# Performance work log

Hardware: AMD Instinct MI355X
Metric: run time of the kernel (lower is better)

## Reference

```python
import jax, jax.numpy as jnp
import numpy as np
import math

B, HW, C, HEADS = 32, 784, 384, 8
T = HW + 1            # 785 tokens incl. cls
TP = HW // 4 + 1      # 197 tokens after pooling
FF = 4 * C
EPS = 1e-5


def _ln2d(x, w, b):
    # nn.LayerNorm over last two dims (tokens, channels) with affine params
    mu = x.mean(axis=(-2, -1), keepdims=True)
    var = x.var(axis=(-2, -1), keepdims=True)
    return (x - mu) / jnp.sqrt(var + EPS) * w + b


def setup_inputs() -> dict:
    key = jax.random.key(0)
    ks = jax.random.split(key, 10)
    sc = math.sqrt(2.0 / C)  # kaiming-ish scale
    rn = lambda k, sh, s=1.0: (jax.random.normal(k, sh, jnp.float32) * s)
    return {
        "x": rn(ks[0], (B, HW, C)),
        "cls_token": rn(ks[1], (B, 1, C)),
        "w_ln1": jnp.ones((T, C), jnp.float32),
        "b_ln1": jnp.zeros((T, C), jnp.float32),
        "Wq": rn(ks[2], (C, C), sc),
        "Wk": rn(ks[3], (C, C), sc),
        "Wv": rn(ks[4], (C, C), sc),
        "Wo": rn(ks[5], (C, C), sc),
        "w_ln2": jnp.ones((TP, C), jnp.float32),
        "b_ln2": jnp.zeros((TP, C), jnp.float32),
        "W1": rn(ks[6], (FF, C), sc),
        "W2": rn(ks[7], (C, FF), math.sqrt(2.0 / FF)),
    }


def reference(x, cls_token, w_ln1, b_ln1, Wq, Wk, Wv, Wo, w_ln2, b_ln2, W1, W2):
    d = C // HEADS
    x_in = jnp.concatenate([cls_token, x], axis=1)           # (B,T,C)
    x1 = _ln2d(x_in, w_ln1, b_ln1)
    # MHSA (dropout disabled for determinism)
    q = (x1 @ Wq.T).reshape(B, T, HEADS, d)
    k = (x1 @ Wk.T).reshape(B, T, HEADS, d)
    v = (x1 @ Wv.T).reshape(B, T, HEADS, d)
    attn = jax.nn.softmax(jnp.einsum('bqhd,bkhd->bhqk', q, k) / math.sqrt(d), axis=-1)
    x_mhsa = jnp.einsum('bhqk,bkhd->bqhd', attn, v).reshape(B, T, C) @ Wo.T
    x_res1 = x_in + x_mhsa
    # Pooling block: channel importance from mean-pooled edge aggregation
    nodes = x_res1[:, 1:]                                     # (B,HW,C)
    ci = jax.nn.sigmoid(x_mhsa.mean(axis=1))                  # (B,C)  AvgPool1d(kernel=T)
    ca = jnp.einsum('bnc,bc->bn', nodes, ci)                  # (B,HW) channel aggregation
    idx = jnp.argsort(ca, axis=1)                             # ascending, like torch.sort
    nodes_sorted = jnp.take_along_axis(nodes, idx[:, :, None], axis=1)
    nodes_pooled = nodes_sorted[:, (HW // 4) * 3:]            # keep top quarter (largest ca)
    x2 = jnp.concatenate([x_res1[:, 0:1], nodes_pooled], axis=1)  # (B,TP,C)
    x2n = _ln2d(x2, w_ln2, b_ln2)
    # MLP (exact-erf GELU, as F.gelu default)
    h = jax.nn.gelu(x2n @ W1.T, approximate=False) @ W2.T
    x_res2 = x2n + h
    return x_res2[:, 1:], x_res2[:, 0:1]
```

## Files before the change

### kernel.cpp

```cpp
#include <hip/hip_runtime.h>
#include <hip/hip_bf16.h>
#include <math.h>

typedef __hip_bfloat16 bf16;
typedef _Float16 f16;
typedef __attribute__((ext_vector_type(8))) _Float16 f16x8;
typedef __attribute__((ext_vector_type(4))) _Float16 f16x4;
typedef __attribute__((ext_vector_type(4))) float f32x4;

#define B_ 32
#define HW_ 784
#define T_ 785
#define TP_ 197
#define C_ 384
#define H_ 8
#define D_ 48
#define FF_ 1536

#define MFMA16(a, b, c) __builtin_amdgcn_mfma_f32_16x16x32_f16(a, b, c, 0, 0, 0)

static constexpr size_t NRES = (size_t)B_ * T_ * C_;
static constexpr size_t NX   = (size_t)B_ * HW_ * C_;
static constexpr size_t NCLS = (size_t)B_ * C_;
static constexpr size_t NLN1 = (size_t)T_ * C_;
static constexpr size_t NWP  = (size_t)C_ * C_;
static constexpr size_t NLN2 = (size_t)TP_ * C_;
static constexpr size_t NW1  = (size_t)FF_ * C_;
static constexpr size_t NX2  = (size_t)B_ * TP_ * C_;
static constexpr size_t NH   = (size_t)B_ * TP_ * FF_;

static constexpr size_t NX1F = (size_t)1576 * 12 * 512;
static constexpr size_t NQKF = (size_t)256 * 56 * 2 * 512;
static constexpr size_t NVF  = (size_t)256 * 3 * 25 * 512;
static constexpr size_t NX2F = (size_t)400 * 12 * 512;
static constexpr size_t NHF  = (size_t)400 * 48 * 512;

static constexpr size_t XF_OFF   = 0;
static constexpr size_t CLSF_OFF = XF_OFF   + NX   * 4;
static constexpr size_t LN1W_OFF = CLSF_OFF + NCLS * 4;
static constexpr size_t LN1B_OFF = LN1W_OFF + NLN1 * 4;
static constexpr size_t WQF_OFF  = LN1B_OFF + NLN1 * 4;
static constexpr size_t LN2W_OFF = WQF_OFF  + 4 * NWP * 4;
static constexpr size_t LN2B_OFF = LN2W_OFF + NLN2 * 4;
static constexpr size_t W1F_OFF  = LN2B_OFF + NLN2 * 4;
static constexpr size_t W2F_OFF  = W1F_OFF  + NW1  * 4;
static constexpr size_t X1H_OFF  = W2F_OFF  + NW1  * 4;
static constexpr size_t X1L_OFF  = X1H_OFF  + NX1F * 2;
static constexpr size_t QFH_OFF  = X1L_OFF  + NX1F * 2;
static constexpr size_t QFL_OFF  = QFH_OFF  + NQKF * 2;
static constexpr size_t KFH_OFF  = QFL_OFF  + NQKF * 2;
static constexpr size_t KFL_OFF  = KFH_OFF  + NQKF * 2;
static constexpr size_t VFH_OFF  = KFL_OFF  + NQKF * 2;
static constexpr size_t VFL_OFF  = VFH_OFF  + NVF  * 2;
static constexpr size_t ATH_OFF  = VFL_OFF  + NVF  * 2;
static constexpr size_t ATL_OFF  = ATH_OFF  + NX1F * 2;
static constexpr size_t XM_OFF   = ATL_OFF  + NX1F * 2;
static constexpr size_t RES_OFF  = XM_OFF   + NRES * 4;
static constexpr size_t X2N_OFF  = RES_OFF  + NRES * 4;
static constexpr size_t X2NH_OFF = X2N_OFF  + NX2  * 4;
static constexpr size_t X2NL_OFF = X2NH_OFF + NX2F * 2;
static constexpr size_t HFH_OFF  = X2NL_OFF + NX2F * 2;
static constexpr size_t HFL_OFF  = HFH_OFF  + NHF  * 2;
static constexpr size_t WPH_OFF  = HFL_OFF  + NHF  * 2;
static constexpr size_t WPL_OFF  = WPH_OFF  + 4 * NWP * 2;
static constexpr size_t WFH_OFF  = WPL_OFF  + 4 * NWP * 2;
static constexpr size_t WFL_OFF  = WFH_OFF  + 2 * NW1 * 2;
static constexpr size_t MU_OFF   = WFL_OFF  + 2 * NW1 * 2;
static constexpr size_t RS_OFF   = MU_OFF   + 128;
static constexpr size_t CID_OFF  = RS_OFF   + 128;
static constexpr size_t CAD_OFF  = CID_OFF  + NCLS * 8;
static constexpr size_t PERM_OFF = CAD_OFF  + (size_t)B_ * HW_ * 8;
static constexpr size_t FLAG_OFF = PERM_OFF + (size_t)B_ * (TP_ - 1) * 4;
static constexpr size_t PS_OFF   = FLAG_OFF + 16;
static constexpr size_t CIP_OFF  = PS_OFF + 32 * 16 * 16;
static constexpr size_t L2PS_OFF = CIP_OFF + (size_t)B_ * 8 * C_ * 8;
static constexpr size_t L2MU_OFF = L2PS_OFF + 32 * 8 * 16;
static constexpr size_t L2RS_OFF = L2MU_OFF + 128;
static constexpr size_t PART_OFF = L2RS_OFF + 128;
static constexpr size_t ARENA_BYTES = PART_OFF + 2 * NX2 * 4;

__device__ __align__(256) unsigned char g_arena[ARENA_BYTES];

template <typename Tp>
__device__ __forceinline__ Tp* ap(size_t off) { return (Tp*)(g_arena + off); }

__device__ __forceinline__ void splitf(float v, f16& h, f16& l)
{
    float a = fabsf(v);
    f16 hv = (a >= 6.103515625e-05f) ? (f16)v : (f16)0.f;
    h = hv;
    l = (f16)((v - (float)hv) * 4096.f);
}

__device__ __forceinline__ size_t afrag(int row, int c, int KC)
{
    return ((size_t)((row >> 4) * KC + (c >> 5)) << 9)
         + (size_t)(((row & 15) | (((c >> 3) & 3) << 4)) << 3) + (c & 7);
}

__global__ void detect_kernel(const unsigned* __restrict__ w)
{
    if (threadIdx.x == 0)
        *ap<int>(FLAG_OFF) = (w[0] == 0x3F803F80u) ? 1 : 0;
}

struct SrcPtrs { const void* p[12]; };
static constexpr size_t SEGB[13] = {
    0,
    NX,
    NX + NCLS,
    NX + NCLS + NLN1,
    NX + NCLS + 2 * NLN1,
    NX + NCLS + 2 * NLN1 + NWP,
    NX + NCLS + 2 * NLN1 + 2 * NWP,
    NX + NCLS + 2 * NLN1 + 3 * NWP,
    NX + NCLS + 2 * NLN1 + 4 * NWP,
    NX + NCLS + 2 * NLN1 + 4 * NWP + NLN2,
    NX + NCLS + 2 * NLN1 + 4 * NWP + 2 * NLN2,
    NX + NCLS + 2 * NLN1 + 4 * NWP + 2 * NLN2 + NW1,
    NX + NCLS + 2 * NLN1 + 4 * NWP + 2 * NLN2 + 2 * NW1,
};
static constexpr size_t NTOT_CVT = SEGB[12];

__global__ __launch_bounds__(256) void cvt_all_kernel(SrcPtrs sp)
{
    size_t i = (size_t)blockIdx.x * 256 + threadIdx.x;
    if (i >= NTOT_CVT) return;
    int seg = 0;
#pragma unroll
    for (int k = 1; k < 12; k++) seg += (i >= SEGB[k]);
    size_t li = i - SEGB[seg];
    const void* src = sp.p[seg];
    float v = (*ap<int>(FLAG_OFF))
        ? __bfloat162float(((const bf16*)src)[li])
        : ((const float*)src)[li];
    ap<float>(XF_OFF)[i] = v;
}

__global__ __launch_bounds__(256) void wrepack_kernel()
{
    size_t i = (size_t)blockIdx.x * 256 + threadIdx.x;
    const size_t n1 = 4 * NWP;
    if (i >= n1 + 2 * NW1) return;
    float v; f16 *oh, *ol;
    if (i < n1) {
        size_t u = i;
        int blk = (int)(u >> 9), le = (int)(u & 511);
        int l = le >> 3, e = le & 7;
        int nt = blk / 12, kc = blk - nt * 12;
        int n = nt * 16 + (l & 15), k = kc * 32 + ((l >> 4) << 3) + e;
        v = ap<float>(WQF_OFF)[(size_t)n * C_ + k];
        oh = ap<f16>(WPH_OFF) + i; ol = ap<f16>(WPL_OFF) + i;
    } else if (i < n1 + NW1) {
        size_t u = i - n1;
        int blk = (int)(u >> 9), le = (int)(u & 511);
        int l = le >> 3, e = le & 7;
        int nt = blk / 12, kc = blk - nt * 12;
        int n = nt * 16 + (l & 15), k = kc * 32 + ((l >> 4) << 3) + e;
        v = ap<float>(W1F_OFF)[(size_t)n * C_ + k];
        oh = ap<f16>(WFH_OFF) + u; ol = ap<f16>(WFL_OFF) + u;
    } else {
        size_t u = i - n1 - NW1;
        int blk = (int)(u >> 9), le = (int)(u & 511);
        int l = le >> 3, e = le & 7;
        int nt = blk / 48, kc = blk - nt * 48;
        int n = nt * 16 + (l & 15), k = kc * 32 + ((l >> 4) << 3) + e;
        v = ap<float>(W2F_OFF)[(size_t)n * FF_ + k];
        oh = ap<f16>(WFH_OFF) + NW1 + u; ol = ap<f16>(WFL_OFF) + NW1 + u;
    }
    f16 h, lo; splitf(v, h, lo);
    *oh = h; *ol = lo;
}

__device__ __forceinline__ float xin_val(int b, int t, int c)
{
    return (t == 0) ? ap<float>(CLSF_OFF)[b * C_ + c]
                    : ap<float>(XF_OFF)[((size_t)b * HW_ + (t - 1)) * C_ + c];
}

__global__ __launch_bounds__(256) void stats1a_kernel()
{
    const int TC = T_ * C_;
    const int SL = (TC + 15) / 16;
    int b = blockIdx.x, s = blockIdx.y, tid = threadIdx.x;
    int e0 = s * SL, e1 = min(e0 + SL, TC);
    __shared__ double r1[256], r2[256];
    double sm = 0.0, s2 = 0.0;
    for (int e = e0 + tid; e < e1; e += 256) {
        int t = e / C_, c = e - t * C_;
        double v = (double)xin_val(b, t, c);
        sm += v; s2 += v * v;
    }
    r1[tid] = sm; r2[tid] = s2; __syncthreads();
    for (int o = 128; o; o >>= 1) {
        if (tid < o) { r1[tid] += r1[tid + o]; r2[tid] += r2[tid + o]; }
        __syncthreads();
    }
    if (tid == 0) {
        double2* ps = ap<double2>(PS_OFF);
        ps[b * 16 + s] = make_double2(r1[0], r2[0]);
    }
}

__global__ __launch_bounds__(64) void stats1b_kernel()
{
    int b = blockIdx.x, lane = threadIdx.x;
    const double2* ps = ap<double2>(PS_OFF);
    double sm = 0.0, s2 = 0.0;
    if (lane < 16) { sm = ps[b * 16 + lane].x; s2 = ps[b * 16 + lane].y; }
    for (int o = 8; o; o >>= 1) { sm += __shfl_down(sm, o); s2 += __shfl_down(s2, o); }
    if (lane == 0) {
        const int TC = T_ * C_;
        double m = sm / TC;
        double var = s2 / TC - m * m;
        ap<float>(MU_OFF)[b] = (float)m;
        ap<float>(RS_OFF)[b] = (float)(1.0 / sqrt(var + 1e-5));
    }
}

__global__ __launch_bounds__(256) void ln1_apply_kernel()
{
    size_t i = (size_t)blockIdx.x * 256 + threadIdx.x;
    if (i >= NRES) return;
    int grow = (int)(i / C_);
    int c = (int)(i - (size_t)grow * C_);
    int b = grow / T_, t = grow - b * T_;
    float v = xin_val(b, t, c);
    float r = (v - ap<float>(MU_OFF)[b]) * ap<float>(RS_OFF)[b]
              * ap<float>(LN1W_OFF)[t * C_ + c]
              + ap<float>(LN1B_OFF)[t * C_ + c];
    f16 h, l; splitf(r, h, l);
    size_t off = afrag(grow, c, 12);
    ap<f16>(X1H_OFF)[off] = h;
    ap<f16>(X1L_OFF)[off] = l;
}

template<int EMODE>
__global__ __launch_bounds__(256, 2) void gemm_fd(
    size_t ah_off, size_t al_off, size_t bh_off, size_t bl_off,
    size_t c_off, int M, int N, int KC, int GY)
{
    int nwg = (int)gridDim.x;
    int lin = blockIdx.x;
    int q8 = nwg >> 3, r8 = nwg & 7, xcd = lin & 7, pos = lin >> 3;
    int wg = (xcd < r8 ? xcd * (q8 + 1) : r8 * (q8 + 1) + (xcd - r8) * q8) + pos;
    int bx = wg / GY, by = wg - bx * GY;
    int kbeg = 0, kend = KC;
    if (EMODE == 6) { int ks = KC >> 1; kbeg = blockIdx.z * ks; kend = kbeg + ks; }
    int tid = threadIdx.x, w = tid >> 6, l = tid & 63;
    int wmt = bx * 8 + (w >> 1) * 4;
    int wnt = by * 8 + (w & 1) * 4;
    const f16* gAh = ap<f16>(ah_off);
    const f16* gAl = ap<f16>(al_off);
    const f16* gBh = ap<f16>(bh_off);
    const f16* gBl = ap<f16>(bl_off);
    size_t ab = (size_t)wmt * KC * 512 + (size_t)l * 8;
    size_t bb = (size_t)wnt * KC * 512 + (size_t)l * 8;

    const f32x4 zf = {0.f, 0.f, 0.f, 0.f};
    f32x4 acc1[4][4], acc2[4][4];
#pragma unroll
    for (int i = 0; i < 4; i++)
#pragma unroll
        for (int j = 0; j < 4; j++) { acc1[i][j] = zf; acc2[i][j] = zf; }

    for (int kc = kbeg; kc < kend; kc++) {
        f16x8 fah[4], fal[4], fbh[4], fbl[4];
#pragma unroll
        for (int i = 0; i < 4; i++) {
            size_t ao = ab + (size_t)(i * KC + kc) * 512;
            size_t bo = bb + (size_t)(i * KC + kc) * 512;
            fah[i] = *(const f16x8*)(gAh + ao);
            fal[i] = *(const f16x8*)(gAl + ao);
            fbh[i] = *(const f16x8*)(gBh + bo);
            fbl[i] = *(const f16x8*)(gBl + bo);
        }
        __builtin_amdgcn_s_setprio(1);
#pragma unroll
        for (int i = 0; i < 4; i++)
#pragma unroll
            for (int j = 0; j < 4; j++) {
                acc1[i][j] = MFMA16(fah[i], fbh[j], acc1[i][j]);
                acc2[i][j] = MFMA16(fah[i], fbl[j], acc2[i][j]);
                acc2[i][j] = MFMA16(fal[i], fbh[j], acc2[i][j]);
            }
        __builtin_amdgcn_s_setprio(0);
    }

    int l4 = ((l >> 4) << 2), lr = l & 15;
#pragma unroll
    for (int i = 0; i < 4; i++) {
        int rowb = (wmt + i) * 16 + l4;
#pragma unroll
        for (int j = 0; j < 4; j++) {
            int col = (wnt + j) * 16 + lr;
#pragma unroll
            for (int r = 0; r < 4; r++) {
                int row = rowb + r;
                if (row >= M) continue;
                float v = acc1[i][j][r] + acc2[i][j][r] * 0.000244140625f;
                if (EMODE == 5) {
                    int seg = col / C_;
                    int cn = col - seg * C_;
                    int hh = cn / D_, dd = cn - hh * D_;
                    int b2 = row / T_, t2 = row - b2 * T_;
                    int bh = b2 * H_ + hh;
                    float vv = (seg == 0) ? v * 0.14433756729740643f : v;
                    f16 h, lo; splitf(vv, h, lo);
                    if (seg < 2) {
                        size_t off = ((size_t)(bh * 112 + (t2 >> 4) * 2 + (dd >> 5)) << 9)
                                   + (size_t)(((t2 & 15) | (((dd >> 3) & 3) << 4)) << 3) + (dd & 7);
                        if (seg == 0) { ap<f16>(QFH_OFF)[off] = h; ap<f16>(QFL_OFF)[off] = lo; }
                        else          { ap<f16>(KFH_OFF)[off] = h; ap<f16>(KFL_OFF)[off] = lo; }
                    } else {
                        size_t off = ((size_t)(bh * 75 + (dd >> 4) * 25 + (t2 >> 5)) << 9)
                                   + (size_t)(((dd & 15) | (((t2 >> 3) & 3) << 4)) << 3) + (t2 & 7);
                        ap<f16>(VFH_OFF)[off] = h; ap<f16>(VFL_OFF)[off] = lo;
                    }
                } else if (EMODE == 4) {
                    ap<float>(c_off)[(size_t)row * N + col] = v;
                    int b2 = row / T_, t2 = row - b2 * T_;
                    ap<float>(RES_OFF)[(size_t)row * N + col] = v + xin_val(b2, t2, col);
                } else if (EMODE == 2) {
                    float g = 0.5f * v * (1.f + erff(v * 0.70710678f));
                    f16 h, lo; splitf(g, h, lo);
                    size_t off = afrag(row, col, 48);
                    ap<f16>(HFH_OFF)[off] = h;
                    ap<f16>(HFL_OFF)[off] = lo;
                } else {
                    ap<float>(PART_OFF)[(size_t)blockIdx.z * NX2 + (size_t)row * N + col] = v;
                }
            }
        }
    }
}

__global__ __launch_bounds__(256) void flash_kernel()
{
    __shared__ f16 Plds[4][2][2][16][40];
    int nwg = (int)gridDim.x;
    int lin = blockIdx.x;
    int q8 = nwg >> 3, r8 = nwg & 7, xcd = lin & 7, pos = lin >> 3;
    int wg = (xcd < r8 ? xcd * (q8 + 1) : r8 * (q8 + 1) + (xcd - r8) * q8) + pos;
    int bh = wg / 7, qblk = wg - bh * 7;
    int wv = threadIdx.x >> 6, l = threadIdx.x & 63;
    int qt0 = qblk * 8 + wv * 2;
    if (qt0 >= 50) return;
    int b = bh >> 3, h = bh & 7;
    size_t qkb = (size_t)bh * 57344;
    const f16* QH = ap<f16>(QFH_OFF) + qkb;
    const f16* QL = ap<f16>(QFL_OFF) + qkb;
    const f16* KH = ap<f16>(KFH_OFF) + qkb;
    const f16* KL = ap<f16>(KFL_OFF) + qkb;
    const f16* VH = ap<f16>(VFH_OFF) + (size_t)bh * 38400;
    const f16* VL = ap<f16>(VFL_OFF) + (size_t)bh * 38400;
    int myq = l & 15, g = l >> 4;

    f16x8 qh[2][2], ql[2][2];
#pragma unroll
    for (int u = 0; u < 2; u++)
#pragma unroll
        for (int kc = 0; kc < 2; kc++) {
            size_t qo = ((size_t)((qt0 + u) * 2 + kc) << 9) + (size_t)l * 8;
            qh[u][kc] = *(const f16x8*)(QH + qo);
            ql[u][kc] = *(const f16x8*)(QL + qo);
        }
    const f32x4 zf = {0.f, 0.f, 0.f, 0.f};
    f32x4 o1[2][3], o2[2][3];
#pragma unroll
    for (int u = 0; u < 2; u++)
#pragma unroll
        for (int j = 0; j < 3; j++) { o1[u][j] = zf; o2[u][j] = zf; }
    float mrun[2] = {-3e38f, -3e38f}, srun[2] = {0.f, 0.f};

    for (int w = 0; w < 25; w++) {
        f16x8 kh[2][2], kl[2][2];
#pragma unroll
        for (int kt2 = 0; kt2 < 2; kt2++)
#pragma unroll
            for (int kc = 0; kc < 2; kc++) {
                size_t ko = ((size_t)((w * 2 + kt2) * 2 + kc) << 9) + (size_t)l * 8;
                kh[kt2][kc] = *(const f16x8*)(KH + ko);
                kl[kt2][kc] = *(const f16x8*)(KL + ko);
            }
        f16x8 vh[3], vl[3];
#pragma unroll
        for (int j = 0; j < 3; j++) {
            size_t vo = ((size_t)(j * 25 + w) << 9) + (size_t)l * 8;
            vh[j] = *(const f16x8*)(VH + vo);
            vl[j] = *(const f16x8*)(VL + vo);
        }
#pragma unroll
        for (int u = 0; u < 2; u++) {
            f32x4 s1[2] = {zf, zf}, s2[2] = {zf, zf};
#pragma unroll
            for (int kt2 = 0; kt2 < 2; kt2++)
#pragma unroll
                for (int kc = 0; kc < 2; kc++) {
                    s1[kt2] = MFMA16(kh[kt2][kc], qh[u][kc], s1[kt2]);
                    s2[kt2] = MFMA16(kh[kt2][kc], ql[u][kc], s2[kt2]);
                    s2[kt2] = MFMA16(kl[kt2][kc], qh[u][kc], s2[kt2]);
                }
            float sv[8];
#pragma unroll
            for (int kt2 = 0; kt2 < 2; kt2++)
#pragma unroll
                for (int r = 0; r < 4; r++)
                    sv[kt2 * 4 + r] = s1[kt2][r] + s2[kt2][r] * 0.000244140625f;
            if (w == 24) {
#pragma unroll
                for (int kt2 = 0; kt2 < 2; kt2++)
#pragma unroll
                    for (int r = 0; r < 4; r++)
                        if (kt2 * 16 + g * 4 + r >= 17) sv[kt2 * 4 + r] = -1e30f;
            }
            float pm = sv[0];
#pragma unroll
            for (int j2 = 1; j2 < 8; j2++) pm = fmaxf(pm, sv[j2]);
            pm = fmaxf(pm, __shfl_xor(pm, 16));
            pm = fmaxf(pm, __shfl_xor(pm, 32));
            float mnew = fmaxf(mrun[u], pm);
            float pv[8]; float ls = 0.f;
#pragma unroll
            for (int j2 = 0; j2 < 8; j2++) { pv[j2] = __expf(sv[j2] - mnew); ls += pv[j2]; }
            ls += __shfl_xor(ls, 16);
            ls += __shfl_xor(ls, 32);
            if (__any(pm > mrun[u])) {
                float fac = __expf(mrun[u] - mnew);
                float fr[4];
#pragma unroll
                for (int r = 0; r < 4; r++) fr[r] = __shfl(fac, g * 4 + r);
#pragma unroll
                for (int j = 0; j < 3; j++)
#pragma unroll
                    for (int r = 0; r < 4; r++) { o1[u][j][r] *= fr[r]; o2[u][j][r] *= fr[r]; }
                srun[u] = srun[u] * fac + ls;
                mrun[u] = mnew;
            } else {
                srun[u] += ls;
            }
#pragma unroll
            for (int kt2 = 0; kt2 < 2; kt2++) {
                f16x4 hh, llo;
#pragma unroll
                for (int r = 0; r < 4; r++) { f16 a, bb2; splitf(pv[kt2 * 4 + r], a, bb2); hh[r] = a; llo[r] = bb2; }
                *(f16x4*)&Plds[wv][u][0][myq][kt2 * 16 + g * 4] = hh;
                *(f16x4*)&Plds[wv][u][1][myq][kt2 * 16 + g * 4] = llo;
            }
            f16x8 pah = *(const f16x8*)&Plds[wv][u][0][myq][g * 8];
            f16x8 pal = *(const f16x8*)&Plds[wv][u][1][myq][g * 8];
#pragma unroll
            for (int j = 0; j < 3; j++) {
                o1[u][j] = MFMA16(pah, vh[j], o1[u][j]);
                o2[u][j] = MFMA16(pah, vl[j], o2[u][j]);
                o2[u][j] = MFMA16(pal, vh[j], o2[u][j]);
            }
        }
    }
#pragma unroll
    for (int u = 0; u < 2; u++) {
        float inv = 1.f / srun[u];
        float ir[4];
#pragma unroll
        for (int r = 0; r < 4; r++) ir[r] = __shfl(inv, g * 4 + r);
#pragma unroll
        for (int j = 0; j < 3; j++) {
            int c = h * D_ + j * 16 + myq;
#pragma unroll
            for (int r = 0; r < 4; r++) {
                int q = (qt0 + u) * 16 + g * 4 + r;
                if (q >= T_) continue;
                float v = (o1[u][j][r] + o2[u][j][r] * 0.000244140625f) * ir[r];
                int grow = b * T_ + q;
                f16 hv, lv; splitf(v, hv, lv);
                size_t off = afrag(grow, c, 12);
                ap<f16>(ATH_OFF)[off] = hv;
                ap<f16>(ATL_OFF)[off] = lv;
            }
        }
    }
}

__global__ __launch_bounds__(384) void cia_kernel()
{
    int b = blockIdx.x, s = blockIdx.y, c = threadIdx.x;
    const float* xm = ap<float>(XM_OFF);
    const int SL = (T_ + 7) / 8;
    int t0 = s * SL, t1 = min(t0 + SL, T_);
    double sm = 0.0;
    for (int t = t0; t < t1; t++) sm += (double)xm[((size_t)b * T_ + t) * C_ + c];
    ap<double>(CIP_OFF)[((size_t)b * 8 + s) * C_ + c] = sm;
}

__global__ __launch_bounds__(384) void cib_kernel()
{
    int b = blockIdx.x, c = threadIdx.x;
    const double* pp = ap<double>(CIP_OFF);
    double sm = 0.0;
#pragma unroll
    for (int s = 0; s < 8; s++) sm += pp[((size_t)b * 8 + s) * C_ + c];
    sm /= (double)T_;
    ap<double>(CID_OFF)[b * C_ + c] = 1.0 / (1.0 + exp(-sm));
}

__global__ __launch_bounds__(64) void ca_kernel()
{
    const float* xres1 = ap<float>(RES_OFF);
    const double* ci   = ap<double>(CID_OFF);
    int idx = blockIdx.x;
    int b = idx / HW_, n = idx - b * HW_;
    int lane = threadIdx.x;
    double s = 0.0;
    for (int c = lane; c < C_; c += 64)
        s += (double)xres1[((size_t)b * T_ + 1 + n) * C_ + c] * ci[b * C_ + c];
    for (int o = 32; o; o >>= 1) s += __shfl_down(s, o);
    if (lane == 0) ap<double>(CAD_OFF)[idx] = s;
}

__global__ __launch_bounds__(256) void rank_kernel()
{
    const double* ca = ap<double>(CAD_OFF);
    int* perm = ap<int>(PERM_OFF);
    int b = blockIdx.x, tid = threadIdx.x;
    __shared__ double cs[HW_];
    for (int i = tid; i < HW_; i += 256) cs[i] = ca[b * HW_ + i];
    __syncthreads();
    for (int i = tid; i < HW_; i += 256) {
        double vi = cs[i];
        int r = 0;
        for (int j = 0; j < HW_; j++) {
            double vj = cs[j];
            r += (vj < vi) || (vj == vi && j < i);
        }
        if (r >= HW_ - TP_ + 1) perm[b * (TP_ - 1) + (r - (HW_ - TP_ + 1))] = i;
    }
}

__global__ __launch_bounds__(256) void ln2a_kernel()
{
    const float* xres1 = ap<float>(RES_OFF);
    const int* perm = ap<int>(PERM_OFF);
    const int TC = TP_ * C_;
    const int SL = (TC + 7) / 8;
    int b = blockIdx.x, s = blockIdx.y, tid = threadIdx.x;
    int e0 = s * SL, e1 = min(e0 + SL, TC);
    __shared__ double r1[256], r2[256];
    double sm = 0.0, s2 = 0.0;
    for (int e = e0 + tid; e < e1; e += 256) {
        int t = e / C_, c = e - t * C_;
        int st = (t == 0) ? 0 : 1 + perm[b * (TP_ - 1) + t - 1];
        double v = (double)xres1[((size_t)b * T_ + st) * C_ + c];
        sm += v; s2 += v * v;
    }
    r1[tid] = sm; r2[tid] = s2; __syncthreads();
    for (int o = 128; o; o >>= 1) {
        if (tid < o) { r1[tid] += r1[tid + o]; r2[tid] += r2[tid + o]; }
        __syncthreads();
    }
    if (tid == 0) {
        double2* ps = ap<double2>(L2PS_OFF);
        ps[b * 8 + s] = make_double2(r1[0], r2[0]);
    }
}

__global__ __launch_bounds__(64) void ln2b_kernel()
{
    int b = blockIdx.x, lane = threadIdx.x;
    const double2* ps = ap<double2>(L2PS_OFF);
    double sm = 0.0, s2 = 0.0;
    if (lane < 8) { sm = ps[b * 8 + lane].x; s2 = ps[b * 8 + lane].y; }
    for (int o = 4; o; o >>= 1) { sm += __shfl_down(sm, o); s2 += __shfl_down(s2, o); }
    if (lane == 0) {
        const int TC = TP_ * C_;
        double m = sm / TC;
        double var = s2 / TC - m * m;
        ap<float>(L2MU_OFF)[b] = (float)m;
        ap<float>(L2RS_OFF)[b] = (float)(1.0 / sqrt(var + 1e-5));
    }
}

__global__ __launch_bounds__(256) void ln2_apply_kernel()
{
    size_t i = (size_t)blockIdx.x * 256 + threadIdx.x;
    if (i >= NX2) return;
    const int TC = TP_ * C_;
    int b = (int)(i / TC);
    int e = (int)(i - (size_t)b * TC);
    int t = e / C_, c = e - t * C_;
    const int* perm = ap<int>(PERM_OFF);
    int st = (t == 0) ? 0 : 1 + perm[b * (TP_ - 1) + t - 1];
    float v = ap<float>(RES_OFF)[((size_t)b * T_ + st) * C_ + c];
    float r = (v - ap<float>(L2MU_OFF)[b]) * ap<float>(L2RS_OFF)[b]
              * ap<float>(LN2W_OFF)[e] + ap<float>(LN2B_OFF)[e];
    ap<float>(X2N_OFF)[i] = r;
    int grow = b * TP_ + t;
    f16 h, l; splitf(r, h, l);
    size_t off = afrag(grow, c, 12);
    ap<f16>(X2NH_OFF)[off] = h;
    ap<f16>(X2NL_OFF)[off] = l;
}

__global__ __launch_bounds__(256) void ffn2_reduce_kernel(float* __restrict__ out)
{
    const size_t tot = NX2;
    size_t i = (size_t)blockIdx.x * 256 + threadIdx.x;
    if (i >= tot) return;
    const float* part = ap<float>(PART_OFF);
    float v = part[i] + part[tot + i] + ap<float>(X2N_OFF)[i];
    int gm = (int)(i / C_);
    int gn = (int)(i - (size_t)gm * C_);
    int b = gm / TP_, t = gm - b * TP_;
    size_t off = (t == 0)
        ? ((size_t)B_ * (TP_ - 1) * C_ + (size_t)b * C_ + gn)
        : ((size_t)(b * (TP_ - 1) + (t - 1)) * C_ + gn);
    out[off] = v;
}

extern "C" void kernel_launch(void* const* d_in, const int* in_sizes, int n_in,
                              void* d_out, int out_size, void* d_ws, size_t ws_size,
                              hipStream_t stream)
{
    float* out = (float*)d_out;
    (void)d_ws; (void)ws_size; (void)in_sizes; (void)n_in; (void)out_size;

    const int M1 = B_ * T_;
    const int M2 = B_ * TP_;

    detect_kernel<<<1, 64, 0, stream>>>((const unsigned*)d_in[2]);
    SrcPtrs sp;
    for (int i = 0; i < 12; i++) sp.p[i] = d_in[i];
    cvt_all_kernel<<<(int)((NTOT_CVT + 255) / 256), 256, 0, stream>>>(sp);
    wrepack_kernel<<<(int)((4 * NWP + 2 * NW1 + 255) / 256), 256, 0, stream>>>();

    stats1a_kernel<<<dim3(B_, 16), 256, 0, stream>>>();
    stats1b_kernel<<<B_, 64, 0, stream>>>();
    ln1_apply_kernel<<<(int)((NRES + 255) / 256), 256, 0, stream>>>();

    gemm_fd<5><<<dim3(197 * 9), 256, 0, stream>>>(
        X1H_OFF, X1L_OFF, WPH_OFF, WPL_OFF, 0, M1, 3 * C_, 12, 9);

    flash_kernel<<<dim3(256 * 7), 256, 0, stream>>>();

    gemm_fd<4><<<dim3(197 * 3), 256, 0, stream>>>(
        ATH_OFF, ATL_OFF,
        WPH_OFF + (size_t)442368 * 2, WPL_OFF + (size_t)442368 * 2,
        XM_OFF, M1, C_, 12, 3);

    cia_kernel<<<dim3(B_, 8), 384, 0, stream>>>();
    cib_kernel<<<B_, 384, 0, stream>>>();
    ca_kernel<<<B_ * HW_, 64, 0, stream>>>();
    rank_kernel<<<B_, 256, 0, stream>>>();
    ln2a_kernel<<<dim3(B_, 8), 256, 0, stream>>>();
    ln2b_kernel<<<B_, 64, 0, stream>>>();
    ln2_apply_kernel<<<(int)((NX2 + 255) / 256), 256, 0, stream>>>();

    gemm_fd<2><<<dim3(50 * 12), 256, 0, stream>>>(
        X2NH_OFF, X2NL_OFF, WFH_OFF, WFL_OFF, 0, M2, FF_, 12, 12);
    gemm_fd<6><<<dim3(50 * 3, 1, 2), 256, 0, stream>>>(
        HFH_OFF, HFL_OFF, WFH_OFF + NW1 * 2, WFL_OFF + NW1 * 2, 0, M2, C_, 48, 3);
    ffn2_reduce_kernel<<<(int)((NX2 + 255) / 256), 256, 0, stream>>>(out);
}
```

Before: 912.8 us.

## Stream V tiles contiguously, add MFMA priority hints, and pack ca_kernel waves

Reorders the V fragment layout so each key window's three tiles sit next to each other, and walks K/V with incrementing pointers. s_setprio is raised around the MFMA bursts in the flash kernel. The max and sum reductions become trees, and the hi/lo split is inlined with a denormal cutoff. ca_kernel now runs four rows per 256-thread block instead of one per 64-thread block, which cuts launch and block overhead. The inlined split could differ slightly from splitf in rounding.

New measurement: 1.072 ms. 1.17x slower.

```diff
diff --git a/kernel.cpp b/kernel.cpp
--- a/kernel.cpp
+++ b/kernel.cpp
@@ -313,7 +313,7 @@
                         if (seg == 0) { ap<f16>(QFH_OFF)[off] = h; ap<f16>(QFL_OFF)[off] = lo; }
                         else          { ap<f16>(KFH_OFF)[off] = h; ap<f16>(KFL_OFF)[off] = lo; }
                     } else {
-                        size_t off = ((size_t)(bh * 75 + (dd >> 4) * 25 + (t2 >> 5)) << 9)
+                        size_t off = ((size_t)(bh * 75 + (t2 >> 5) * 3 + (dd >> 4)) << 9)
                                    + (size_t)(((dd & 15) | (((t2 >> 3) & 3) << 4)) << 3) + (t2 & 7);
                         ap<f16>(VFH_OFF)[off] = h; ap<f16>(VFL_OFF)[off] = lo;
                     }
@@ -350,10 +350,10 @@
     size_t qkb = (size_t)bh * 57344;
     const f16* QH = ap<f16>(QFH_OFF) + qkb;
     const f16* QL = ap<f16>(QFL_OFF) + qkb;
-    const f16* KH = ap<f16>(KFH_OFF) + qkb;
-    const f16* KL = ap<f16>(KFL_OFF) + qkb;
-    const f16* VH = ap<f16>(VFH_OFF) + (size_t)bh * 38400;
-    const f16* VL = ap<f16>(VFL_OFF) + (size_t)bh * 38400;
+    const f16* kptrH = ap<f16>(KFH_OFF) + qkb + (size_t)l * 8;
+    const f16* kptrL = ap<f16>(KFL_OFF) + qkb + (size_t)l * 8;
+    const f16* vptrH = ap<f16>(VFH_OFF) + (size_t)bh * 38400 + (size_t)l * 8;
+    const f16* vptrL = ap<f16>(VFL_OFF) + (size_t)bh * 38400 + (size_t)l * 8;
     int myq = l & 15, g = l >> 4;
 
     f16x8 qh[2][2], ql[2][2];
@@ -374,33 +374,34 @@
     float mrun[2] = {-3e38f, -3e38f}, srun[2] = {0.f, 0.f};
 
     for (int w = 0; w < 25; w++) {
-        f16x8 kh[2][2], kl[2][2];
-#pragma unroll
-        for (int kt2 = 0; kt2 < 2; kt2++)
-#pragma unroll
-            for (int kc = 0; kc < 2; kc++) {
-                size_t ko = ((size_t)((w * 2 + kt2) * 2 + kc) << 9) + (size_t)l * 8;
-                kh[kt2][kc] = *(const f16x8*)(KH + ko);
-                kl[kt2][kc] = *(const f16x8*)(KL + ko);
-            }
+        f16x8 kh[4], kl[4];
+#pragma unroll
+        for (int t = 0; t < 4; t++) {
+            kh[t] = *(const f16x8*)(kptrH + t * 512);
+            kl[t] = *(const f16x8*)(kptrL + t * 512);
+        }
+        kptrH += 2048; kptrL += 2048;
         f16x8 vh[3], vl[3];
 #pragma unroll
         for (int j = 0; j < 3; j++) {
-            size_t vo = ((size_t)(j * 25 + w) << 9) + (size_t)l * 8;
-            vh[j] = *(const f16x8*)(VH + vo);
-            vl[j] = *(const f16x8*)(VL + vo);
-        }
+            vh[j] = *(const f16x8*)(vptrH + j * 512);
+            vl[j] = *(const f16x8*)(vptrL + j * 512);
+        }
+        vptrH += 1536; vptrL += 1536;
 #pragma unroll
         for (int u = 0; u < 2; u++) {
             f32x4 s1[2] = {zf, zf}, s2[2] = {zf, zf};
+            __builtin_amdgcn_s_setprio(1);
 #pragma unroll
             for (int kt2 = 0; kt2 < 2; kt2++)
 #pragma unroll
                 for (int kc = 0; kc < 2; kc++) {
-                    s1[kt2] = MFMA16(kh[kt2][kc], qh[u][kc], s1[kt2]);
-                    s2[kt2] = MFMA16(kh[kt2][kc], ql[u][kc], s2[kt2]);
-                    s2[kt2] = MFMA16(kl[kt2][kc], qh[u][kc], s2[kt2]);
+                    int t = kt2 * 2 + kc;
+                    s1[kt2] = MFMA16(kh[t], qh[u][kc], s1[kt2]);
+                    s2[kt2] = MFMA16(kh[t], ql[u][kc], s2[kt2]);
+                    s2[kt2] = MFMA16(kl[t], qh[u][kc], s2[kt2]);
                 }
+            __builtin_amdgcn_s_setprio(0);
             float sv[8];
 #pragma unroll
             for (int kt2 = 0; kt2 < 2; kt2++)
@@ -414,15 +415,16 @@
                     for (int r = 0; r < 4; r++)
                         if (kt2 * 16 + g * 4 + r >= 17) sv[kt2 * 4 + r] = -1e30f;
             }
-            float pm = sv[0];
-#pragma unroll
-            for (int j2 = 1; j2 < 8; j2++) pm = fmaxf(pm, sv[j2]);
+            float pm = fmaxf(fmaxf(fmaxf(sv[0], sv[1]), fmaxf(sv[2], sv[3])),
+                             fmaxf(fmaxf(sv[4], sv[5]), fmaxf(sv[6], sv[7])));
             pm = fmaxf(pm, __shfl_xor(pm, 16));
             pm = fmaxf(pm, __shfl_xor(pm, 32));
             float mnew = fmaxf(mrun[u], pm);
-            float pv[8]; float ls = 0.f;
-#pragma unroll
-            for (int j2 = 0; j2 < 8; j2++) { pv[j2] = __expf(sv[j2] - mnew); ls += pv[j2]; }
+            float pv[8];
+#pragma unroll
+            for (int j2 = 0; j2 < 8; j2++) pv[j2] = __expf(sv[j2] - mnew);
+            float ls = ((pv[0] + pv[1]) + (pv[2] + pv[3]))
+                     + ((pv[4] + pv[5]) + (pv[6] + pv[7]));
             ls += __shfl_xor(ls, 16);
             ls += __shfl_xor(ls, 32);
             if (__any(pm > mrun[u])) {
@@ -443,18 +445,25 @@
             for (int kt2 = 0; kt2 < 2; kt2++) {
                 f16x4 hh, llo;
 #pragma unroll
-                for (int r = 0; r < 4; r++) { f16 a, bb2; splitf(pv[kt2 * 4 + r], a, bb2); hh[r] = a; llo[r] = bb2; }
+                for (int r = 0; r < 4; r++) {
+                    float pvv = pv[kt2 * 4 + r];
+                    f16 a = (pvv >= 6.103515625e-05f) ? (f16)pvv : (f16)0.f;
+                    hh[r] = a;
+                    llo[r] = (f16)((pvv - (float)a) * 4096.f);
+                }
                 *(f16x4*)&Plds[wv][u][0][myq][kt2 * 16 + g * 4] = hh;
                 *(f16x4*)&Plds[wv][u][1][myq][kt2 * 16 + g * 4] = llo;
             }
             f16x8 pah = *(const f16x8*)&Plds[wv][u][0][myq][g * 8];
             f16x8 pal = *(const f16x8*)&Plds[wv][u][1][myq][g * 8];
+            __builtin_amdgcn_s_setprio(1);
 #pragma unroll
             for (int j = 0; j < 3; j++) {
                 o1[u][j] = MFMA16(pah, vh[j], o1[u][j]);
                 o2[u][j] = MFMA16(pah, vl[j], o2[u][j]);
                 o2[u][j] = MFMA16(pal, vh[j], o2[u][j]);
             }
+            __builtin_amdgcn_s_setprio(0);
         }
     }
 #pragma unroll
@@ -503,13 +512,13 @@
     ap<double>(CID_OFF)[b * C_ + c] = 1.0 / (1.0 + exp(-sm));
 }
 
-__global__ __launch_bounds__(64) void ca_kernel()
+__global__ __launch_bounds__(256) void ca_kernel()
 {
     const float* xres1 = ap<float>(RES_OFF);
     const double* ci   = ap<double>(CID_OFF);
-    int idx = blockIdx.x;
+    int idx = blockIdx.x * 4 + (threadIdx.x >> 6);
     int b = idx / HW_, n = idx - b * HW_;
-    int lane = threadIdx.x;
+    int lane = threadIdx.x & 63;
     double s = 0.0;
     for (int c = lane; c < C_; c += 64)
         s += (double)xres1[((size_t)b * T_ + 1 + n) * C_ + c] * ci[b * C_ + c];
@@ -648,7 +657,7 @@
 
     cia_kernel<<<dim3(B_, 8), 384, 0, stream>>>();
     cib_kernel<<<B_, 384, 0, stream>>>();
-    ca_kernel<<<B_ * HW_, 64, 0, stream>>>();
+    ca_kernel<<<B_ * HW_ / 4, 256, 0, stream>>>();
     rank_kernel<<<B_, 256, 0, stream>>>();
     ln2a_kernel<<<dim3(B_, 8), 256, 0, stream>>>();
     ln2b_kernel<<<B_, 64, 0, stream>>>();
```
